# Kernel optimization log

Hardware: AMD Instinct MI355X
Metric: run time of the kernel (lower is better)

## Reference

```python
import jax, jax.numpy as jnp
import numpy as np

# Static dims (chosen so check_image_size padding is a no-op)
B, C, H, W = 4, 96, 256, 256
NUM_HEADS = 4
WIN_PARAM = 8          # number of windows per dim
SUB = 4                # sub-window pixel size
WIN_H = H // WIN_PARAM  # 32: window pixel size
WIN_W = W // WIN_PARAM
SCALE = (C // NUM_HEADS) ** -0.5


def setup_inputs() -> dict:
    key = jax.random.key(0)
    ks = jax.random.split(key, 4)
    s = 0.02
    return {
        "x": jax.random.normal(ks[0], (B, C, H, W), jnp.float32),
        "q_w": jax.random.normal(ks[1], (C, C), jnp.float32) * s,
        "q_b": jnp.zeros((C,), jnp.float32),
        "kv_w": jax.random.normal(ks[2], (2 * C, C), jnp.float32) * s,
        "kv_b": jnp.zeros((2 * C,), jnp.float32),
        "proj_w": jax.random.normal(ks[3], (C, C), jnp.float32) * s,
        "proj_b": jnp.zeros((C,), jnp.float32),
    }


def reference(x, q_w, q_b, kv_w, kv_b, proj_w, proj_b):
    nWh, nWw = H // WIN_H, W // WIN_W
    nW = nWh * nWw                      # 64 windows
    swh, sww = WIN_H // SUB, WIN_W // SUB
    sNW = swh * sww                     # 64 sub-windows per window
    N = SUB * SUB                       # 16 tokens per sub-window
    d = C // NUM_HEADS

    # B C (nWh wH) (nWw wW) -> B nW wH wW C
    wx = x.reshape(B, C, nWh, WIN_H, nWw, WIN_W).transpose(0, 2, 4, 3, 5, 1)
    wx = wx.reshape(B, nW, WIN_H, WIN_W, C)
    # B nW (swh sub)(sww sub) C -> B nW sNW N C
    sx = wx.reshape(B, nW, swh, SUB, sww, SUB, C).transpose(0, 1, 2, 4, 3, 5, 6)
    sx = sx.reshape(B, nW, sNW, N, C)
    # shuffle: B sNW nW N C
    sh = sx.transpose(0, 2, 1, 3, 4)
    pooled = sh.mean(axis=3)                     # B sNW nW C
    merged = sh.reshape(B, sNW, nW * N, C)       # B sNW (nW N) C

    q = pooled @ q_w.T + q_b                     # B sNW nW C
    kv = merged @ kv_w.T + kv_b                  # B sNW nW*N 2C
    k, v = kv[..., :C], kv[..., C:]

    q = q.reshape(B, sNW, nW, NUM_HEADS, d).transpose(0, 1, 3, 2, 4) * SCALE
    k = k.reshape(B, sNW, nW * N, NUM_HEADS, d).transpose(0, 1, 3, 2, 4)
    v = v.reshape(B, sNW, nW * N, NUM_HEADS, d).transpose(0, 1, 3, 2, 4)

    attn = jax.nn.softmax(jnp.einsum('bshqd,bshkd->bshqk', q, k), axis=-1)
    o = jnp.einsum('bshqk,bshkd->bshqd', attn, v)          # B sNW nH nW d

    # B sNW nH nW d -> B nW sNW (nH d)
    o = o.transpose(0, 3, 1, 2, 4).reshape(B, nW, sNW, C)
    o = o @ proj_w.T + proj_b

    # broadcast each sub-window result to its N tokens (repeat)
    o = jnp.broadcast_to(o[:, :, :, None, :], (B, nW, sNW, N, C))
    # B nW (swh sww)(sub sub) C -> B nW wH wW C
    o = o.reshape(B, nW, swh, sww, SUB, SUB, C).transpose(0, 1, 2, 4, 3, 5, 6)
    o = o.reshape(B, nW, WIN_H, WIN_W, C)
    # B (nWh nWw) wH wW C -> B C H W
    o = o.reshape(B, nWh, nWw, WIN_H, WIN_W, C).transpose(0, 5, 1, 3, 2, 4)
    return o.reshape(B, C, H, W)
```

## Files before the change

### kernel.cpp

```cpp
#include <hip/hip_runtime.h>
#include <hip/hip_bf16.h>
#include <stdint.h>

#define PLANE 65536
#define SCALE_F 0.20412414523193154f

typedef __attribute__((ext_vector_type(8))) short short8;
typedef __attribute__((ext_vector_type(4))) float f32x4;

__device__ __forceinline__ unsigned pk2(float a, float b) {
  union { __hip_bfloat162 h; unsigned u; } cv;
  cv.h = __float22bfloat162_rn(make_float2(a, b));
  return cv.u;
}

__global__ __launch_bounds__(256) void prep_kernel(
    const float* __restrict__ kvw, unsigned short* __restrict__ w_a1,
    unsigned short* __restrict__ w_b2) {
  int tid = blockIdx.x * 256 + threadIdx.x;
  int side = tid / 1536;
  int r = tid % 1536;
  int frag = r >> 6;
  int lane = r & 63;
  int tile = frag / 3, ks = frag % 3;
  int od = tile * 16 + (lane & 15);
  int c0 = ks * 32 + (lane >> 4) * 8;
  int h = od >> 5, dd = od & 31;
  unsigned out[4] = {0u, 0u, 0u, 0u};
  if (dd < 24) {
    int row = (side == 0) ? (h * 24 + dd) : (96 + h * 24 + dd);
    const float* src = kvw + row * 96 + c0;
    float4 f0 = *(const float4*)src;
    float4 f1 = *(const float4*)(src + 4);
    out[0] = pk2(f0.x, f0.y); out[1] = pk2(f0.z, f0.w);
    out[2] = pk2(f1.x, f1.y); out[3] = pk2(f1.z, f1.w);
  }
  unsigned* dst =
      (unsigned*)((side == 0) ? w_a1 : w_b2) + (frag * 64 + lane) * 4;
  dst[0] = out[0]; dst[1] = out[1]; dst[2] = out[2]; dst[3] = out[3];
}

__global__ __launch_bounds__(512) void tp_kernel(const float* __restrict__ x,
                                                 unsigned short* __restrict__ xT,
                                                 float* __restrict__ pooled) {
  __shared__ unsigned Lq[48 * 128];
  int blk = blockIdx.x;
  int h = blk & 1;
  int swr = (blk >> 1) & 7;
  int wh = (blk >> 4) & 7;
  int b = blk >> 7;
  int t = threadIdx.x;
  int c4l = t & 31;
  int cpg = t >> 5;
  int ka = c4l >> 3;

  float pacc[3][2];
  #pragma unroll
  for (int j = 0; j < 3; ++j) { pacc[j][0] = 0.f; pacc[j][1] = 0.f; }

  for (int pr = 0; pr < 4; ++pr) {
    int r = wh * 32 + swr * 4 + pr;
    const float* xrow =
        x + ((size_t)(b * 96) * 256 + r) * 256 + (h * 32 + c4l) * 4;
    #pragma unroll
    for (int j = 0; j < 3; ++j) {
      int cpair = j * 16 + cpg;
      int cg = cpair >> 2;
      const float* pA = xrow + (size_t)(2 * cpair) * PLANE;
      float4 vA = *(const float4*)pA;
      float4 vB = *(const float4*)(pA + PLANE);
      pacc[j][0] += (vA.x + vA.y) + (vA.z + vA.w);
      pacc[j][1] += (vB.x + vB.y) + (vB.z + vB.w);
      unsigned w0 = pk2(vA.x, vB.x), w1 = pk2(vA.y, vB.y);
      unsigned w2 = pk2(vA.z, vB.z), w3 = pk2(vA.w, vB.w);
      int K = ka | ((cg & 7) << 2);
      int base = cpair * 128;
      int c0 = 4 * c4l;
      Lq[base + ((c0 + 0) ^ K)] = w0;
      Lq[base + ((c0 + 1) ^ K)] = w1;
      Lq[base + ((c0 + 2) ^ K)] = w2;
      Lq[base + ((c0 + 3) ^ K)] = w3;
    }
    __syncthreads();
    uint4* dst = (uint4*)xT + (size_t)(b * 256 + r) * 3072;
    #pragma unroll
    for (int it = 0; it < 3; ++it) {
      int id = it * 512 + t;
      int ckl = id / 12;
      int cg = id - ckl * 12;
      int sw = ckl >> 4, pw = (ckl >> 2) & 3, wwl = ckl & 3;
      int coll = wwl * 32 + sw * 4 + pw;
      int K = wwl | ((cg & 7) << 2);
      int cx = coll ^ K;
      unsigned q0 = Lq[(cg * 4 + 0) * 128 + cx];
      unsigned q1 = Lq[(cg * 4 + 1) * 128 + cx];
      unsigned q2 = Lq[(cg * 4 + 2) * 128 + cx];
      unsigned q3 = Lq[(cg * 4 + 3) * 128 + cx];
      int colkey = sw * 32 + pw * 8 + h * 4 + wwl;
      dst[colkey * 12 + cg] = make_uint4(q0, q1, q2, q3);
    }
    __syncthreads();
  }
  int sw = c4l & 7, ww = h * 4 + (c4l >> 3);
  #pragma unroll
  for (int j = 0; j < 3; ++j)
    #pragma unroll
    for (int e = 0; e < 2; ++e) {
      int ch = 2 * (j * 16 + cpg) + e;
      pooled[(((size_t)(b * 64 + swr * 8 + sw)) * 96 + ch) * 64 + wh * 8 + ww] =
          pacc[j][e] * 0.0625f;
    }
}

__global__ __launch_bounds__(256) void qgemm_kernel(
    const float* __restrict__ pooled, const float* __restrict__ qw,
    const float* __restrict__ qb, float* __restrict__ q_ws) {
  __shared__ float pl[64 * 97];
  int blk = blockIdx.x;
  int cog = blk & 3, bs = blk >> 2;
  int t = threadIdx.x;
  const float* src = pooled + (size_t)bs * 6144;
  #pragma unroll
  for (int k = 0; k < 24; ++k) {
    int idx = t + k * 256;
    int c = idx >> 6, w = idx & 63;
    pl[w * 97 + c] = src[idx];
  }
  __syncthreads();
  int wv = t >> 6, lane = t & 63;
  float acc[6] = {0.f, 0.f, 0.f, 0.f, 0.f, 0.f};
  const float* qwr = qw + (cog * 24 + wv) * 96;
  #pragma unroll 4
  for (int c = 0; c < 96; ++c) {
    float v = pl[lane * 97 + c];
    #pragma unroll
    for (int k = 0; k < 6; ++k) acc[k] += v * qwr[k * 384 + c];
  }
  #pragma unroll
  for (int k = 0; k < 6; ++k) {
    int co = cog * 24 + k * 4 + wv;
    q_ws[((size_t)bs * 64 + lane) * 96 + co] = (acc[k] + qb[co]) * SCALE_F;
  }
}

__global__ __launch_bounds__(512, 2) void attn_kernel(
    const unsigned short* __restrict__ xT,
    const unsigned short* __restrict__ w_a1,
    const unsigned short* __restrict__ w_b2, const float* __restrict__ kvb,
    const float* __restrict__ q_ws, float* __restrict__ o_ws) {
  extern __shared__ __align__(16) char sm[];
  char* Xs = sm;
  char* Ks = sm + 32768;
  char* Vs = sm + 59392;
  char* Ps = sm + 94208;
  float* lbuf = (float*)sm;

  int bs = blockIdx.x;
  int b = bs >> 6, s = bs & 63;
  int sh = s >> 3, sw = s & 7;
  int t = threadIdx.x;
  int w = t >> 6, lane = t & 63;
  int l15 = lane & 15, quad = lane >> 4;

  int mhA1 = w >> 2, nhA1 = w & 3;
  int mhA2 = w & 3, nhA2 = w >> 2;
  int head = w & 3, khalf = w >> 2;
  int nh = w >> 2;

  short8 wa[4][3], wb[4][3];
  #pragma unroll
  for (int i = 0; i < 4; ++i)
    #pragma unroll
    for (int k = 0; k < 3; ++k) {
      wa[i][k] = *(const short8*)(w_a1 + (((4 * mhA1 + i) * 3 + k) * 64 + lane) * 8);
      wb[i][k] = *(const short8*)(w_b2 + (((4 * nhA2 + i) * 3 + k) * 64 + lane) * 8);
    }

  short8 qf[4];
  #pragma unroll
  for (int nt = 0; nt < 4; ++nt) {
    short8 f = {0, 0, 0, 0, 0, 0, 0, 0};
    if (quad < 3) {
      const float* qp =
          q_ws + ((size_t)bs * 64 + nt * 16 + l15) * 96 + head * 24 + quad * 8;
      float4 a = *(const float4*)qp;
      float4 c = *(const float4*)(qp + 4);
      union { short8 s8; unsigned u[4]; } cv;
      cv.u[0] = pk2(a.x, a.y); cv.u[1] = pk2(a.z, a.w);
      cv.u[2] = pk2(c.x, c.y); cv.u[3] = pk2(c.z, c.w);
      f = cv.s8;
    }
    qf[nt] = f;
  }

  float bK[4][4];
  #pragma unroll
  for (int i = 0; i < 4; ++i) {
    int od0 = (4 * mhA1 + i) * 16 + quad * 4;
    #pragma unroll
    for (int r = 0; r < 4; ++r) {
      int od = od0 + r, dd = od & 31, h = od >> 5;
      bK[i][r] = (dd < 24) ? kvb[h * 24 + dd] : 0.f;
    }
  }
  float bV[4];
  #pragma unroll
  for (int i = 0; i < 4; ++i) {
    int vd = (4 * nhA2 + i) * 16 + l15, dd = vd & 31, h = vd >> 5;
    bV[i] = (dd < 24) ? kvb[96 + h * 24 + dd] : 0.f;
  }

  f32x4 zz = {0.f, 0.f, 0.f, 0.f};
  f32x4 oacc[2][2];
  #pragma unroll
  for (int m = 0; m < 2; ++m)
    #pragma unroll
    for (int n = 0; n < 2; ++n) oacc[m][n] = zz;
  float lacc[4] = {0.f, 0.f, 0.f, 0.f};

  const char* sb0 = (const char*)xT + (((size_t)(b * 256 + sh * 4) * 8 + sw) * 6144);

  for (int ti = 0; ti < 8; ++ti) {
    const char* sb = sb0 + (size_t)ti * 32 * 8 * 6144;
    #pragma unroll
    for (int i = 0; i < 3; ++i) {
      int l = i * 512 + t;
      int pr = l / 384;
      int rem = l - pr * 384;
      int key = pr * 32 + rem / 12;
      int c = rem - (rem / 12) * 12;
      uint4 v = *(const uint4*)(sb + (size_t)pr * 49152 + (size_t)rem * 16);
      *(uint4*)(Xs + key * 256 + ((c ^ (key & 7)) << 4)) = v;
    }
    __syncthreads();

    {
      f32x4 acc[4][2];
      #pragma unroll
      for (int i = 0; i < 4; ++i)
        #pragma unroll
        for (int n = 0; n < 2; ++n) {
          f32x4 a; a.x = bK[i][0]; a.y = bK[i][1]; a.z = bK[i][2]; a.w = bK[i][3];
          acc[i][n] = a;
        }
      short8 bx[2][3];
      #pragma unroll
      for (int n = 0; n < 2; ++n) {
        int key = (2 * nhA1 + n) * 16 + l15;
        #pragma unroll
        for (int k = 0; k < 3; ++k)
          bx[n][k] = *(const short8*)(Xs + key * 256 +
                                      (((k * 4 + quad) ^ (key & 7)) << 4));
      }
      #pragma unroll
      for (int i = 0; i < 4; ++i)
        #pragma unroll
        for (int n = 0; n < 2; ++n)
          #pragma unroll
          for (int k = 0; k < 3; ++k)
            acc[i][n] = __builtin_amdgcn_mfma_f32_16x16x32_bf16(
                wa[i][k], bx[n][k], acc[i][n], 0, 0, 0);
      #pragma unroll
      for (int i = 0; i < 4; ++i) {
        int od0 = (4 * mhA1 + i) * 16 + quad * 4;
        int dd0 = od0 & 31;
        if (dd0 < 24) {
          int h = od0 >> 5;
          #pragma unroll
          for (int n = 0; n < 2; ++n) {
            int key = (2 * nhA1 + n) * 16 + l15;
            *(int2*)(Ks + key * 208 + (h * 24 + dd0) * 2) =
                make_int2(pk2(acc[i][n].x, acc[i][n].y),
                          pk2(acc[i][n].z, acc[i][n].w));
          }
        }
      }
    }

    {
      short8 ax[2][3];
      #pragma unroll
      for (int m = 0; m < 2; ++m) {
        int key = (2 * mhA2 + m) * 16 + l15;
        #pragma unroll
        for (int k = 0; k < 3; ++k)
          ax[m][k] = *(const short8*)(Xs + key * 256 +
                                      (((k * 4 + quad) ^ (key & 7)) << 4));
      }
      #pragma unroll
      for (int m = 0; m < 2; ++m)
        #pragma unroll
        for (int n = 0; n < 4; ++n) {
          f32x4 acc; acc.x = bV[n]; acc.y = bV[n]; acc.z = bV[n]; acc.w = bV[n];
          #pragma unroll
          for (int k = 0; k < 3; ++k)
            acc = __builtin_amdgcn_mfma_f32_16x16x32_bf16(ax[m][k], wb[n][k],
                                                          acc, 0, 0, 0);
          int vd = (4 * nhA2 + n) * 16 + l15;
          int key0 = (2 * mhA2 + m) * 16 + quad * 4;
          *(int2*)(Vs + vd * 272 + key0 * 2) =
              make_int2(pk2(acc.x, acc.y), pk2(acc.z, acc.w));
        }
    }
    __syncthreads();

    {
      f32x4 sa[4][4];
      #pragma unroll
      for (int mt = 0; mt < 4; ++mt)
        #pragma unroll
        for (int nt = 0; nt < 4; ++nt) sa[mt][nt] = zz;
      #pragma unroll
      for (int mt = 0; mt < 4; ++mt) {
        int key = khalf * 64 + mt * 16 + l15;
        short8 ak = {0, 0, 0, 0, 0, 0, 0, 0};
        if (quad < 3)
          ak = *(const short8*)(Ks + key * 208 + head * 48 + quad * 16);
        #pragma unroll
        for (int nt = 0; nt < 4; ++nt)
          sa[mt][nt] = __builtin_amdgcn_mfma_f32_16x16x32_bf16(ak, qf[nt],
                                                               sa[mt][nt], 0, 0, 0);
      }
      #pragma unroll
      for (int mt = 0; mt < 4; ++mt) {
        int key0 = khalf * 64 + mt * 16 + quad * 4;
        #pragma unroll
        for (int nt = 0; nt < 4; ++nt) {
          float e0 = __expf(sa[mt][nt].x), e1 = __expf(sa[mt][nt].y);
          float e2 = __expf(sa[mt][nt].z), e3 = __expf(sa[mt][nt].w);
          lacc[nt] += (e0 + e1) + (e2 + e3);
          *(int2*)(Ps + head * 17408 + (nt * 16 + l15) * 272 + key0 * 2) =
              make_int2(pk2(e0, e1), pk2(e2, e3));
        }
      }
      if (ti == 7) {
        #pragma unroll
        for (int nt = 0; nt < 4; ++nt) {
          float v = lacc[nt];
          v += __shfl_xor(v, 16);
          v += __shfl_xor(v, 32);
          if (quad == 0) lbuf[(head * 2 + khalf) * 64 + nt * 16 + l15] = v;
        }
      }
    }
    __syncthreads();

    #pragma unroll
    for (int ks = 0; ks < 4; ++ks) {
      short8 av[2];
      #pragma unroll
      for (int mt = 0; mt < 2; ++mt)
        av[mt] = *(const short8*)(Vs + (head * 32 + mt * 16 + l15) * 272 +
                                  ks * 64 + quad * 16);
      #pragma unroll
      for (int n = 0; n < 2; ++n) {
        short8 bp = *(const short8*)(Ps + head * 17408 +
                                     ((2 * nh + n) * 16 + l15) * 272 +
                                     ks * 64 + quad * 16);
        #pragma unroll
        for (int mt = 0; mt < 2; ++mt)
          oacc[mt][n] = __builtin_amdgcn_mfma_f32_16x16x32_bf16(av[mt], bp,
                                                                oacc[mt][n], 0, 0, 0);
      }
    }
  }

  #pragma unroll
  for (int n = 0; n < 2; ++n) {
    int q = (2 * nh + n) * 16 + l15;
    float l = lbuf[(head * 2 + 0) * 64 + q] + lbuf[(head * 2 + 1) * 64 + q];
    float inv = 1.0f / l;
    #pragma unroll
    for (int mt = 0; mt < 2; ++mt)
      #pragma unroll
      for (int r = 0; r < 4; ++r) {
        int d = mt * 16 + quad * 4 + r;
        if (d < 24)
          o_ws[((size_t)bs * 64 + q) * 96 + head * 24 + d] = oacc[mt][n][r] * inv;
      }
  }
}

__global__ __launch_bounds__(256) void proj_kernel(const float* __restrict__ o_ws,
                                                   const float* __restrict__ pw,
                                                   const float* __restrict__ pb,
                                                   float* __restrict__ out) {
  __shared__ float ol[64 * 97];
  int blk = blockIdx.x;
  int cog = blk & 3, sh = (blk >> 2) & 7, wh = (blk >> 5) & 7, b = blk >> 8;
  int t = threadIdx.x;

  #pragma unroll
  for (int k = 0; k < 24; ++k) {
    int id = k * 256 + t;
    int pair = id / 96, c = id - pair * 96;
    int sw = pair >> 3, ww = pair & 7;
    ol[pair * 97 + c] =
        o_ws[(((size_t)(b * 64 + sh * 8 + sw)) * 64 + wh * 8 + ww) * 96 + c];
  }
  __syncthreads();

  int wv = t >> 6, lane = t & 63;
  int pair = (lane & 7) * 8 + (lane >> 3);
  float acc[6] = {0.f, 0.f, 0.f, 0.f, 0.f, 0.f};
  const float* pwr = pw + (cog * 24 + wv) * 96;
  #pragma unroll 4
  for (int c = 0; c < 96; ++c) {
    float v = ol[pair * 97 + c];
    #pragma unroll
    for (int k = 0; k < 6; ++k) acc[k] += v * pwr[k * 384 + c];
  }

  #pragma unroll
  for (int k = 0; k < 6; ++k) {
    int co = cog * 24 + k * 4 + wv;
    float val = acc[k] + pb[co];
    float4 pk = make_float4(val, val, val, val);
    size_t rowbase = ((size_t)(b * 96 + co) * 256 + wh * 32 + sh * 4) * 256;
    #pragma unroll
    for (int ph = 0; ph < 4; ++ph)
      *(float4*)(out + rowbase + ph * 256 + lane * 4) = pk;
  }
}

extern "C" void kernel_launch(void* const* d_in, const int* in_sizes, int n_in,
                              void* d_out, int out_size, void* d_ws,
                              size_t ws_size, hipStream_t stream) {
  const float* x = (const float*)d_in[0];
  const float* qw = (const float*)d_in[1];
  const float* qb = (const float*)d_in[2];
  const float* kvw = (const float*)d_in[3];
  const float* kvb = (const float*)d_in[4];
  const float* pw = (const float*)d_in[5];
  const float* pb = (const float*)d_in[6];

  float* pooled = (float*)d_ws;
  float* q_ws = pooled + 1572864;
  float* o_ws = q_ws + 1572864;
  unsigned short* w_a1 = (unsigned short*)(o_ws + 1572864);
  unsigned short* w_b2 = w_a1 + 12288;
  unsigned short* xT = w_b2 + 12288;

  static int attn_lds = 163840;
  (void)hipFuncSetAttribute((const void*)attn_kernel,
                            hipFuncAttributeMaxDynamicSharedMemorySize,
                            attn_lds);

  hipLaunchKernelGGL(prep_kernel, dim3(12), dim3(256), 0, stream, kvw, w_a1, w_b2);
  hipLaunchKernelGGL(tp_kernel, dim3(512), dim3(512), 0, stream, x, xT, pooled);
  hipLaunchKernelGGL(qgemm_kernel, dim3(1024), dim3(256), 0, stream, pooled, qw,
                     qb, q_ws);
  hipLaunchKernelGGL(attn_kernel, dim3(256), dim3(512), attn_lds, stream, xT,
                     w_a1, w_b2, kvb, q_ws, o_ws);
  hipLaunchKernelGGL(proj_kernel, dim3(1024), dim3(256), 0, stream, o_ws, pw, pb,
                     (float*)d_out);
}
```

Baseline: 297.9 us.

## Split transpose kernel per row with partial pools; prefetch xT tiles in attention

```diff
diff --git a/kernel.cpp b/kernel.cpp
--- a/kernel.cpp
+++ b/kernel.cpp
@@ -4,6 +4,7 @@
 
 #define PLANE 65536
 #define SCALE_F 0.20412414523193154f
+#define PPART 1572864
 
 typedef __attribute__((ext_vector_type(8))) short short8;
 typedef __attribute__((ext_vector_type(4))) float f32x4;
@@ -42,89 +43,92 @@
 
 __global__ __launch_bounds__(512) void tp_kernel(const float* __restrict__ x,
                                                  unsigned short* __restrict__ xT,
-                                                 float* __restrict__ pooled) {
+                                                 float* __restrict__ pooled_part) {
   __shared__ unsigned Lq[48 * 128];
   int blk = blockIdx.x;
   int h = blk & 1;
-  int swr = (blk >> 1) & 7;
-  int wh = (blk >> 4) & 7;
-  int b = blk >> 7;
+  int pr = (blk >> 1) & 3;
+  int swr = (blk >> 3) & 7;
+  int wh = (blk >> 6) & 7;
+  int b = blk >> 9;
   int t = threadIdx.x;
   int c4l = t & 31;
   int cpg = t >> 5;
   int ka = c4l >> 3;
 
+  int r = wh * 32 + swr * 4 + pr;
+  const float* xrow =
+      x + ((size_t)(b * 96) * 256 + r) * 256 + (h * 32 + c4l) * 4;
+
   float pacc[3][2];
   #pragma unroll
-  for (int j = 0; j < 3; ++j) { pacc[j][0] = 0.f; pacc[j][1] = 0.f; }
-
-  for (int pr = 0; pr < 4; ++pr) {
-    int r = wh * 32 + swr * 4 + pr;
-    const float* xrow =
-        x + ((size_t)(b * 96) * 256 + r) * 256 + (h * 32 + c4l) * 4;
-    #pragma unroll
-    for (int j = 0; j < 3; ++j) {
-      int cpair = j * 16 + cpg;
-      int cg = cpair >> 2;
-      const float* pA = xrow + (size_t)(2 * cpair) * PLANE;
-      float4 vA = *(const float4*)pA;
-      float4 vB = *(const float4*)(pA + PLANE);
-      pacc[j][0] += (vA.x + vA.y) + (vA.z + vA.w);
-      pacc[j][1] += (vB.x + vB.y) + (vB.z + vB.w);
-      unsigned w0 = pk2(vA.x, vB.x), w1 = pk2(vA.y, vB.y);
-      unsigned w2 = pk2(vA.z, vB.z), w3 = pk2(vA.w, vB.w);
-      int K = ka | ((cg & 7) << 2);
-      int base = cpair * 128;
-      int c0 = 4 * c4l;
-      Lq[base + ((c0 + 0) ^ K)] = w0;
-      Lq[base + ((c0 + 1) ^ K)] = w1;
-      Lq[base + ((c0 + 2) ^ K)] = w2;
-      Lq[base + ((c0 + 3) ^ K)] = w3;
-    }
-    __syncthreads();
-    uint4* dst = (uint4*)xT + (size_t)(b * 256 + r) * 3072;
-    #pragma unroll
-    for (int it = 0; it < 3; ++it) {
-      int id = it * 512 + t;
-      int ckl = id / 12;
-      int cg = id - ckl * 12;
-      int sw = ckl >> 4, pw = (ckl >> 2) & 3, wwl = ckl & 3;
-      int coll = wwl * 32 + sw * 4 + pw;
-      int K = wwl | ((cg & 7) << 2);
-      int cx = coll ^ K;
-      unsigned q0 = Lq[(cg * 4 + 0) * 128 + cx];
-      unsigned q1 = Lq[(cg * 4 + 1) * 128 + cx];
-      unsigned q2 = Lq[(cg * 4 + 2) * 128 + cx];
-      unsigned q3 = Lq[(cg * 4 + 3) * 128 + cx];
-      int colkey = sw * 32 + pw * 8 + h * 4 + wwl;
-      dst[colkey * 12 + cg] = make_uint4(q0, q1, q2, q3);
-    }
-    __syncthreads();
-  }
-  int sw = c4l & 7, ww = h * 4 + (c4l >> 3);
-  #pragma unroll
-  for (int j = 0; j < 3; ++j)
-    #pragma unroll
-    for (int e = 0; e < 2; ++e) {
-      int ch = 2 * (j * 16 + cpg) + e;
-      pooled[(((size_t)(b * 64 + swr * 8 + sw)) * 96 + ch) * 64 + wh * 8 + ww] =
-          pacc[j][e] * 0.0625f;
-    }
+  for (int j = 0; j < 3; ++j) {
+    int cpair = j * 16 + cpg;
+    int cg = cpair >> 2;
+    const float* pA = xrow + (size_t)(2 * cpair) * PLANE;
+    float4 vA = *(const float4*)pA;
+    float4 vB = *(const float4*)(pA + PLANE);
+    pacc[j][0] = (vA.x + vA.y) + (vA.z + vA.w);
+    pacc[j][1] = (vB.x + vB.y) + (vB.z + vB.w);
+    unsigned w0 = pk2(vA.x, vB.x), w1 = pk2(vA.y, vB.y);
+    unsigned w2 = pk2(vA.z, vB.z), w3 = pk2(vA.w, vB.w);
+    int K = ka | ((cg & 7) << 2);
+    int base = cpair * 128;
+    int c0 = 4 * c4l;
+    Lq[base + ((c0 + 0) ^ K)] = w0;
+    Lq[base + ((c0 + 1) ^ K)] = w1;
+    Lq[base + ((c0 + 2) ^ K)] = w2;
+    Lq[base + ((c0 + 3) ^ K)] = w3;
+  }
+
+  {
+    int sw = c4l & 7, ww = h * 4 + (c4l >> 3);
+    float* pp = pooled_part + (size_t)pr * PPART;
+    #pragma unroll
+    for (int j = 0; j < 3; ++j)
+      #pragma unroll
+      for (int e = 0; e < 2; ++e) {
+        int ch = 2 * (j * 16 + cpg) + e;
+        pp[(((size_t)(b * 64 + swr * 8 + sw)) * 96 + ch) * 64 + wh * 8 + ww] =
+            pacc[j][e];
+      }
+  }
+  __syncthreads();
+
+  uint4* dst = (uint4*)xT + (size_t)(b * 256 + r) * 3072;
+  #pragma unroll
+  for (int it = 0; it < 3; ++it) {
+    int id = it * 512 + t;
+    int ckl = id / 12;
+    int cg = id - ckl * 12;
+    int sw = ckl >> 4, pw = (ckl >> 2) & 3, wwl = ckl & 3;
+    int coll = wwl * 32 + sw * 4 + pw;
+    int K = wwl | ((cg & 7) << 2);
+    int cx = coll ^ K;
+    unsigned q0 = Lq[(cg * 4 + 0) * 128 + cx];
+    unsigned q1 = Lq[(cg * 4 + 1) * 128 + cx];
+    unsigned q2 = Lq[(cg * 4 + 2) * 128 + cx];
+    unsigned q3 = Lq[(cg * 4 + 3) * 128 + cx];
+    int colkey = sw * 32 + pw * 8 + h * 4 + wwl;
+    dst[colkey * 12 + cg] = make_uint4(q0, q1, q2, q3);
+  }
 }
 
 __global__ __launch_bounds__(256) void qgemm_kernel(
-    const float* __restrict__ pooled, const float* __restrict__ qw,
+    const float* __restrict__ pooled_part, const float* __restrict__ qw,
     const float* __restrict__ qb, float* __restrict__ q_ws) {
   __shared__ float pl[64 * 97];
   int blk = blockIdx.x;
   int cog = blk & 3, bs = blk >> 2;
   int t = threadIdx.x;
-  const float* src = pooled + (size_t)bs * 6144;
+  const float* src = pooled_part + (size_t)bs * 6144;
   #pragma unroll
   for (int k = 0; k < 24; ++k) {
     int idx = t + k * 256;
     int c = idx >> 6, w = idx & 63;
-    pl[w * 97 + c] = src[idx];
+    float v = (src[idx] + src[idx + PPART]) +
+              (src[idx + 2 * PPART] + src[idx + 3 * PPART]);
+    pl[w * 97 + c] = v * 0.0625f;
   }
   __syncthreads();
   int wv = t >> 6, lane = t & 63;
@@ -220,18 +224,24 @@
 
   const char* sb0 = (const char*)xT + (((size_t)(b * 256 + sh * 4) * 8 + sw) * 6144);
 
+  int off_g[3], off_l[3];
+  #pragma unroll
+  for (int i = 0; i < 3; ++i) {
+    int l = i * 512 + t;
+    int pr = l / 384;
+    int rem = l - pr * 384;
+    int key = pr * 32 + rem / 12;
+    int c = rem - (rem / 12) * 12;
+    off_g[i] = pr * 49152 + rem * 16;
+    off_l[i] = key * 256 + ((c ^ (key & 7)) << 4);
+  }
+  uint4 stg[3];
+  #pragma unroll
+  for (int i = 0; i < 3; ++i) stg[i] = *(const uint4*)(sb0 + off_g[i]);
+
   for (int ti = 0; ti < 8; ++ti) {
-    const char* sb = sb0 + (size_t)ti * 32 * 8 * 6144;
-    #pragma unroll
-    for (int i = 0; i < 3; ++i) {
-      int l = i * 512 + t;
-      int pr = l / 384;
-      int rem = l - pr * 384;
-      int key = pr * 32 + rem / 12;
-      int c = rem - (rem / 12) * 12;
-      uint4 v = *(const uint4*)(sb + (size_t)pr * 49152 + (size_t)rem * 16);
-      *(uint4*)(Xs + key * 256 + ((c ^ (key & 7)) << 4)) = v;
-    }
+    #pragma unroll
+    for (int i = 0; i < 3; ++i) *(uint4*)(Xs + off_l[i]) = stg[i];
     __syncthreads();
 
     {
@@ -304,6 +314,12 @@
     }
     __syncthreads();
 
+    if (ti < 7) {
+      const char* sb = sb0 + (size_t)(ti + 1) * 32 * 8 * 6144;
+      #pragma unroll
+      for (int i = 0; i < 3; ++i) stg[i] = *(const uint4*)(sb + off_g[i]);
+    }
+
     {
       f32x4 sa[4][4];
       #pragma unroll
@@ -434,10 +450,10 @@
   const float* pw = (const float*)d_in[5];
   const float* pb = (const float*)d_in[6];
 
-  float* pooled = (float*)d_ws;
-  float* q_ws = pooled + 1572864;
-  float* o_ws = q_ws + 1572864;
-  unsigned short* w_a1 = (unsigned short*)(o_ws + 1572864);
+  float* pooled_part = (float*)d_ws;
+  float* q_ws = pooled_part + 4 * PPART;
+  float* o_ws = q_ws + PPART;
+  unsigned short* w_a1 = (unsigned short*)(o_ws + PPART);
   unsigned short* w_b2 = w_a1 + 12288;
   unsigned short* xT = w_b2 + 12288;
 
@@ -447,9 +463,10 @@
                             attn_lds);
 
   hipLaunchKernelGGL(prep_kernel, dim3(12), dim3(256), 0, stream, kvw, w_a1, w_b2);
-  hipLaunchKernelGGL(tp_kernel, dim3(512), dim3(512), 0, stream, x, xT, pooled);
-  hipLaunchKernelGGL(qgemm_kernel, dim3(1024), dim3(256), 0, stream, pooled, qw,
-                     qb, q_ws);
+  hipLaunchKernelGGL(tp_kernel, dim3(2048), dim3(512), 0, stream, x, xT,
+                     pooled_part);
+  hipLaunchKernelGGL(qgemm_kernel, dim3(1024), dim3(256), 0, stream, pooled_part,
+                     qw, qb, q_ws);
   hipLaunchKernelGGL(attn_kernel, dim3(256), dim3(512), attn_lds, stream, xT,
                      w_a1, w_b2, kvb, q_ws, o_ws);
   hipLaunchKernelGGL(proj_kernel, dim3(1024), dim3(256), 0, stream, o_ws, pw, pb,
```

New measurement: 318.7 us. 7.0% more time.
